# Kernel optimization log

Hardware: AMD Instinct MI355X
Metric: run time of the kernel (lower is better)

The kernel has to match this reference:

```python
import jax, jax.numpy as jnp
import numpy as np

N = 200000
E = 3200000
EPS = 1e-5


def setup_inputs() -> dict:
    key = jax.random.key(0)
    ks = jax.random.split(key, 8)
    x = jax.random.normal(ks[0], (N, 128), dtype=jnp.float32)
    edge_index = jax.random.randint(ks[1], (2, E), 0, N, dtype=jnp.int32)
    def lin(k, fi, fo):
        s = 1.0 / np.sqrt(fi)
        return jax.random.uniform(k, (fi, fo), jnp.float32, -s, s)
    return {
        "x": x,
        "edge_index": edge_index,
        "W1": lin(ks[2], 128, 256), "b1": jnp.zeros((256,), jnp.float32),
        "gamma1": jnp.ones((256,), jnp.float32), "beta1": jnp.zeros((256,), jnp.float32),
        "W2": lin(ks[3], 256, 256), "b2": jnp.zeros((256,), jnp.float32),
        "gamma2": jnp.ones((256,), jnp.float32), "beta2": jnp.zeros((256,), jnp.float32),
        "W3": lin(ks[4], 256, 40), "b3": jnp.zeros((40,), jnp.float32),
    }


def _gcn_norm(edge_index):
    # add self-loops, compute symmetric GCN normalization
    loop = jnp.arange(N, dtype=jnp.int32)
    row = jnp.concatenate([edge_index[0], loop])
    col = jnp.concatenate([edge_index[1], loop])
    deg = jax.ops.segment_sum(jnp.ones_like(row, dtype=jnp.float32), row, num_segments=N)
    dinv = jax.lax.rsqrt(jnp.maximum(deg, 1.0))  # deg >= 1 due to self-loops
    norm = dinv[row] * dinv[col]  # [E+N]
    return row, col, norm


def _gcn_conv(x, W, b, row, col, norm):
    h = x @ W                                  # [N, Fout] small GEMM
    msg = h[col] * norm[:, None]               # gather + scale  [E+N, Fout]
    out = jax.ops.segment_sum(msg, row, num_segments=N)  # scatter-add
    return out + b


def _batchnorm(x, gamma, beta):
    mu = jnp.mean(x, axis=0)
    var = jnp.var(x, axis=0)
    return (x - mu) * jax.lax.rsqrt(var + EPS) * gamma + beta


def reference(x, edge_index, W1, b1, gamma1, beta1, W2, b2, gamma2, beta2, W3, b3):
    row, col, norm = _gcn_norm(edge_index)
    h = _gcn_conv(x, W1, b1, row, col, norm)
    h = jax.nn.relu(_batchnorm(h, gamma1, beta1))
    h = _gcn_conv(h, W2, b2, row, col, norm)
    h = jax.nn.relu(_batchnorm(h, gamma2, beta2))
    h = _gcn_conv(h, W3, b3, row, col, norm)
    return jax.nn.log_softmax(h, axis=-1)
```

## Files before the change

### kernel.cpp

```cpp
#include <hip/hip_runtime.h>
#include <hip/hip_bf16.h>

#define NNODES 200000
#define NEDGES 3200000
#define NBUCK 782
#define NEB 512
#define EPB (NEDGES / NEB)
#define EPS 1e-5f
#define AGGB_CHUNK 50000
#define AGGF_CHUNK 100000

typedef __bf16 bf16x8 __attribute__((ext_vector_type(8)));
typedef float  f32x4  __attribute__((ext_vector_type(4)));
typedef float  f32x2  __attribute__((ext_vector_type(2)));

__device__ __forceinline__ float bflo(unsigned u) { return __uint_as_float(u << 16); }
__device__ __forceinline__ float bfhi(unsigned u) { return __uint_as_float(u & 0xffff0000u); }
__device__ __forceinline__ unsigned short f2b(float f) {
    return __builtin_bit_cast(unsigned short, __float2bfloat16(f));
}
__device__ __forceinline__ unsigned pk2(float a, float b) {
    return (unsigned)f2b(a) | ((unsigned)f2b(b) << 16);
}
__device__ __forceinline__ unsigned bnrelu_pk(unsigned u, f32x2 c, f32x2 h) {
    f32x2 v = { __uint_as_float(u << 16), __uint_as_float(u & 0xffff0000u) };
    v = __builtin_elementwise_fma(v, c, h);
    const f32x2 z = {0.f, 0.f};
    v = __builtin_elementwise_max(v, z);
    return pk2(v[0], v[1]);
}

__device__ __forceinline__ void prepw_one(const float* __restrict__ W,
                                          unsigned short* __restrict__ Wswz,
                                          int K, int NOUT, int t) {
    int KSTEPS = K / 32;
    int lane = t & 63;
    int ks = (t >> 6) % KSTEPS;
    int g  = (t >> 6) / KSTEPS;
    int c = lane & 15, q = lane >> 4;
    int col = g * 16 + c;
    int k0 = ks * 32 + q * 8;
    unsigned short vals[8];
#pragma unroll
    for (int j = 0; j < 8; ++j)
        vals[j] = (col < NOUT) ? f2b(W[(size_t)(k0 + j) * NOUT + col]) : (unsigned short)0;
    *(uint4*)((char*)Wswz + (size_t)t * 16) = __builtin_bit_cast(uint4, vals);
}

__global__ __launch_bounds__(256) void k_cnt(const int* __restrict__ row, int* __restrict__ cnt,
                                             const float* __restrict__ W1,
                                             const float* __restrict__ W2,
                                             const float* __restrict__ W3,
                                             unsigned short* __restrict__ w1s,
                                             unsigned short* __restrict__ w2s,
                                             unsigned short* __restrict__ w3s,
                                             unsigned* __restrict__ statsz) {
    const int blk = blockIdx.x;
    if (blk == NEB + 54) {
        for (int i = threadIdx.x; i < 1026; i += 256) statsz[i] = 0u;
        return;
    }
    if (blk >= NEB) {
        int t = (blk - NEB) * 256 + threadIdx.x;
        if (t < 4096) prepw_one(W1, w1s, 128, 256, t);
        else if (t < 12288) prepw_one(W2, w2s, 256, 256, t - 4096);
        else if (t < 13824) prepw_one(W3, w3s, 256, 40, t - 12288);
        return;
    }
    __shared__ int h[NBUCK];
    for (int i = threadIdx.x; i < NBUCK; i += 256) h[i] = 0;
    __syncthreads();
    const int e0 = blk * EPB;
    for (int i = e0 + threadIdx.x; i < e0 + EPB; i += 256)
        atomicAdd(&h[row[i] >> 8], 1);
    __syncthreads();
    for (int i = threadIdx.x; i < NBUCK; i += 256)
        cnt[(size_t)blk * NBUCK + i] = h[i];
}

__global__ __launch_bounds__(256) void k_bscan(int* __restrict__ cnt, int* __restrict__ btot) {
    const int wv = (blockIdx.x * 256 + threadIdx.x) >> 6;
    const int lane = threadIdx.x & 63;
    if (wv >= NBUCK) return;
    int v[8]; int s = 0;
#pragma unroll
    for (int j = 0; j < 8; ++j) {
        v[j] = cnt[(size_t)(lane * 8 + j) * NBUCK + wv];
        s += v[j];
    }
    int excl = s;
#pragma unroll
    for (int o = 1; o < 64; o <<= 1) {
        int t = __shfl_up(excl, o);
        if (lane >= o) excl += t;
    }
    excl -= s;
    if (lane == 63) btot[wv] = excl + s;
    int base = excl;
#pragma unroll
    for (int j = 0; j < 8; ++j) {
        int t = v[j];
        cnt[(size_t)(lane * 8 + j) * NBUCK + wv] = base;
        base += t;
    }
}

__global__ __launch_bounds__(256) void k_place(const int* __restrict__ row, const int* __restrict__ col,
                                               const int* __restrict__ cnt, const int* __restrict__ btot,
                                               int* __restrict__ bbase, unsigned* __restrict__ ebuf) {
    __shared__ int sbb[NBUCK];
    __shared__ int tp[256];
    __shared__ int base[NBUCK];
    const int t = threadIdx.x;
    int v[4]; int loc = 0;
    const int i0 = t * 4;
#pragma unroll
    for (int j = 0; j < 4; ++j) {
        int idx = i0 + j;
        v[j] = (idx < NBUCK) ? btot[idx] : 0;
        loc += v[j];
    }
    tp[t] = loc;
    __syncthreads();
    for (int off = 1; off < 256; off <<= 1) {
        int u = (t >= off) ? tp[t - off] : 0;
        __syncthreads();
        tp[t] += u;
        __syncthreads();
    }
    int run = tp[t] - loc;
#pragma unroll
    for (int j = 0; j < 4; ++j) {
        int idx = i0 + j;
        if (idx < NBUCK) sbb[idx] = run;
        run += v[j];
    }
    __syncthreads();
    if (blockIdx.x == 0) {
        for (int i = t; i < NBUCK; i += 256) bbase[i] = sbb[i];
        if (t == 0) bbase[NBUCK] = NEDGES;
    }
    for (int i = t; i < NBUCK; i += 256)
        base[i] = sbb[i] + cnt[(size_t)blockIdx.x * NBUCK + i];
    __syncthreads();
    const int e0 = blockIdx.x * EPB;
    for (int i = e0 + t; i < e0 + EPB; i += 256) {
        int r = row[i], c = col[i];
        int p = atomicAdd(&base[r >> 8], 1);
        ebuf[p] = ((unsigned)(r & 255) << 18) | (unsigned)c;
    }
}

__global__ __launch_bounds__(256) void k_sort2(const unsigned* __restrict__ ebuf,
                                               const int* __restrict__ bbase,
                                               int* __restrict__ offs, float* __restrict__ dinv,
                                               int* __restrict__ csr,
                                               const float* __restrict__ x,
                                               uint4* __restrict__ xb) {
    __shared__ int cnt[256];
    __shared__ int sofs[256];
    __shared__ int sc[256];
    __shared__ float sdinv[256];
    const int b = blockIdx.x;
    const int t = threadIdx.x;
    const int n0 = b * 256;
    cnt[t] = 0;
    __syncthreads();
    const int s = bbase[b], e = bbase[b + 1];
    for (int i = s + t; i < e; i += 256)
        atomicAdd(&cnt[ebuf[i] >> 18], 1);
    __syncthreads();
    const int c = cnt[t];
    sc[t] = c;
    __syncthreads();
    for (int off = 1; off < 256; off <<= 1) {
        int v = (t >= off) ? sc[t - off] : 0;
        __syncthreads();
        sc[t] += v;
        __syncthreads();
    }
    const int excl = sc[t] - c;
    sofs[t] = s + excl;
    const int n = n0 + t;
    float dv = rsqrtf((float)(c + 1));
    sdinv[t] = dv;
    if (n < NNODES) {
        offs[n] = s + excl;
        dinv[n] = dv;
    }
    if (b == NBUCK - 1 && t == 0) offs[NNODES] = NEDGES;
    cnt[t] = 0;
    __syncthreads();
    for (int i = s + t; i < e; i += 256) {
        unsigned v = ebuf[i];
        int nl = v >> 18;
        int rank = atomicAdd(&cnt[nl], 1);
        csr[sofs[nl] + rank] = (int)(v & 0x3FFFFu);
    }
    const int nn = (NNODES - n0 < 256) ? (NNODES - n0) : 256;
    const float4* xp = (const float4*)(x + (size_t)n0 * 128);
    uint4* xo = xb + (size_t)n0 * 16;
    const int lim = nn * 16;
    for (int i = t; i < lim; i += 256) {
        float d = sdinv[i >> 4];
        float4 a = xp[i * 2], bb = xp[i * 2 + 1];
        uint4 o;
        o.x = pk2(a.x * d, a.y * d);  o.y = pk2(a.z * d, a.w * d);
        o.z = pk2(bb.x * d, bb.y * d); o.w = pk2(bb.z * d, bb.w * d);
        xo[i] = o;
    }
}

__global__ __launch_bounds__(256) void k_aggf(const uint4* __restrict__ in,
                                              const int* __restrict__ offs,
                                              const int* __restrict__ csr,
                                              const float* __restrict__ dinv,
                                              uint4* __restrict__ out,
                                              int nbase) {
    const int lane = threadIdx.x & 63;
    const int grp = lane >> 4;
    const int fl = lane & 15;
    const int node = nbase + blockIdx.x * 4 + (threadIdx.x >> 6);
    const int p0 = offs[node];
    const int K = offs[node + 1] - p0 + 1;
    float a0=0,a1=0,a2=0,a3=0,a4=0,a5=0,a6=0,a7=0;
    auto accum = [&](uint4 u) {
        a0 += bflo(u.x); a1 += bfhi(u.x);
        a2 += bflo(u.y); a3 += bfhi(u.y);
        a4 += bflo(u.z); a5 += bfhi(u.z);
        a6 += bflo(u.w); a7 += bfhi(u.w);
    };
    int k = 0;
    for (; k + 16 <= K; k += 16) {
        int j0 = k + grp;
        int i0 = (j0 == 0) ? node : csr[p0 + j0 - 1];
        int i1 = csr[p0 + k + 3 + grp];
        int i2 = csr[p0 + k + 7 + grp];
        int i3 = csr[p0 + k + 11 + grp];
        uint4 u0 = in[(size_t)i0 * 16 + fl];
        uint4 u1 = in[(size_t)i1 * 16 + fl];
        uint4 u2 = in[(size_t)i2 * 16 + fl];
        uint4 u3 = in[(size_t)i3 * 16 + fl];
        accum(u0); accum(u1); accum(u2); accum(u3);
    }
    for (; k + 8 <= K; k += 8) {
        int j0 = k + grp;
        int i0 = (j0 == 0) ? node : csr[p0 + j0 - 1];
        int i1 = csr[p0 + k + 3 + grp];
        uint4 u0 = in[(size_t)i0 * 16 + fl];
        uint4 u1 = in[(size_t)i1 * 16 + fl];
        accum(u0); accum(u1);
    }
    for (; k + 4 <= K; k += 4) {
        int j0 = k + grp;
        int i0 = (j0 == 0) ? node : csr[p0 + j0 - 1];
        accum(in[(size_t)i0 * 16 + fl]);
    }
    int rem = K - k;
    if (grp < rem) {
        int j0 = k + grp;
        int i0 = (j0 == 0) ? node : csr[p0 + j0 - 1];
        accum(in[(size_t)i0 * 16 + fl]);
    }
#define RED(v) v += __shfl_xor(v, 32); v += __shfl_xor(v, 16);
    RED(a0) RED(a1) RED(a2) RED(a3) RED(a4) RED(a5) RED(a6) RED(a7)
#undef RED
    if (grp == 0) {
        const float d = dinv[node];
        uint4 o;
        o.x = pk2(a0 * d, a1 * d); o.y = pk2(a2 * d, a3 * d);
        o.z = pk2(a4 * d, a5 * d); o.w = pk2(a6 * d, a7 * d);
        out[(size_t)node * 16 + fl] = o;
    }
}

__global__ __launch_bounds__(256) void k_aggb(const uint4* __restrict__ in,
                                              const int* __restrict__ offs,
                                              const int* __restrict__ csr,
                                              const float* __restrict__ dinv,
                                              uint4* __restrict__ out,
                                              int nbase) {
    const int lane = threadIdx.x & 63;
    const int half = lane >> 5;
    const int fl = lane & 31;
    const int node = nbase + blockIdx.x * 4 + (threadIdx.x >> 6);
    const int p0 = offs[node];
    const int K = offs[node + 1] - p0 + 1;
    float a0=0,a1=0,a2=0,a3=0,a4=0,a5=0,a6=0,a7=0;
    auto accum = [&](uint4 u) {
        a0 += bflo(u.x); a1 += bfhi(u.x);
        a2 += bflo(u.y); a3 += bfhi(u.y);
        a4 += bflo(u.z); a5 += bfhi(u.z);
        a6 += bflo(u.w); a7 += bfhi(u.w);
    };
    auto idxAt = [&](int j) -> int { return (j == 0) ? node : csr[p0 + j - 1]; };
    int k = 0;
    for (; k + 8 <= K; k += 8) {
        int i0 = idxAt(k + half);
        int i1 = csr[p0 + k + 1 + half];
        int i2 = csr[p0 + k + 3 + half];
        int i3 = csr[p0 + k + 5 + half];
        uint4 u0 = in[(size_t)i0 * 32 + fl];
        uint4 u1 = in[(size_t)i1 * 32 + fl];
        uint4 u2 = in[(size_t)i2 * 32 + fl];
        uint4 u3 = in[(size_t)i3 * 32 + fl];
        accum(u0); accum(u1); accum(u2); accum(u3);
    }
    for (; k + 2 <= K; k += 2) {
        accum(in[(size_t)idxAt(k + half) * 32 + fl]);
    }
    if (k < K && half == 0) {
        accum(in[(size_t)idxAt(k) * 32 + fl]);
    }
#define RED(v) v += __shfl_xor(v, 32);
    RED(a0) RED(a1) RED(a2) RED(a3) RED(a4) RED(a5) RED(a6) RED(a7)
#undef RED
    if (half == 0) {
        const float d = dinv[node];
        uint4 o;
        o.x = pk2(a0 * d, a1 * d); o.y = pk2(a2 * d, a3 * d);
        o.z = pk2(a4 * d, a5 * d); o.w = pk2(a6 * d, a7 * d);
        out[(size_t)node * 32 + fl] = o;
    }
}

__global__ __launch_bounds__(256) void k_agg3(const uint4* __restrict__ T3b,
                                              const int* __restrict__ offs,
                                              const int* __restrict__ csr,
                                              const float* __restrict__ dinv,
                                              const float* __restrict__ b3,
                                              float* __restrict__ out) {
    const int lane = threadIdx.x & 63;
    const int grp = lane / 5;
    const int fl = lane - grp * 5;
    const bool act = grp < 12;
    const int node = blockIdx.x * 4 + (threadIdx.x >> 6);
    const int p0 = offs[node];
    const int K = offs[node + 1] - p0 + 1;
    float a0=0,a1=0,a2=0,a3=0,a4=0,a5=0,a6=0,a7=0;
    auto accum = [&](uint4 u) {
        a0 += bflo(u.x); a1 += bfhi(u.x);
        a2 += bflo(u.y); a3 += bfhi(u.y);
        a4 += bflo(u.z); a5 += bfhi(u.z);
        a6 += bflo(u.w); a7 += bfhi(u.w);
    };
    const char* Tb = (const char*)T3b;
    int k = 0;
    if (act) {
        for (; k + 12 <= K; k += 12) {
            int j = k + grp;
            int i0 = (j == 0) ? node : csr[p0 + j - 1];
            accum(*(const uint4*)(Tb + (size_t)i0 * 128 + fl * 16));
        }
        int rem = K - k;
        if (grp < rem) {
            int j = k + grp;
            int i0 = (j == 0) ? node : csr[p0 + j - 1];
            accum(*(const uint4*)(Tb + (size_t)i0 * 128 + fl * 16));
        }
    }
#define RED3(v) { float t = __shfl(v, lane + 30); v += t; t = __shfl(v, lane + 15); v += t; \
                  float u1 = __shfl(v, lane + 5); float u2 = __shfl(v, lane + 10); v += u1 + u2; }
    RED3(a0) RED3(a1) RED3(a2) RED3(a3) RED3(a4) RED3(a5) RED3(a6) RED3(a7)
#undef RED3
    const float d = dinv[node];
    float v[8];
    if (grp == 0) {
        const float4* bp = (const float4*)(b3 + fl * 8);
        float4 b01 = bp[0], b23 = bp[1];
        v[0] = a0 * d + b01.x; v[1] = a1 * d + b01.y;
        v[2] = a2 * d + b01.z; v[3] = a3 * d + b01.w;
        v[4] = a4 * d + b23.x; v[5] = a5 * d + b23.y;
        v[6] = a6 * d + b23.z; v[7] = a7 * d + b23.w;
    } else {
#pragma unroll
        for (int j = 0; j < 8; ++j) v[j] = -INFINITY;
    }
    float m = v[0];
#pragma unroll
    for (int j = 1; j < 8; ++j) m = fmaxf(m, v[j]);
    float mm = __shfl(m, 0);
#pragma unroll
    for (int l = 1; l < 5; ++l) mm = fmaxf(mm, __shfl(m, l));
    float e = 0.f;
    if (grp == 0) {
#pragma unroll
        for (int j = 0; j < 8; ++j) e += __expf(v[j] - mm);
    }
    float s = __shfl(e, 0);
#pragma unroll
    for (int l = 1; l < 5; ++l) s += __shfl(e, l);
    float ls = __logf(s);
    if (grp == 0) {
        float* op = out + (size_t)node * 40 + fl * 8;
        float4 o0 = {v[0] - mm - ls, v[1] - mm - ls, v[2] - mm - ls, v[3] - mm - ls};
        float4 o1 = {v[4] - mm - ls, v[5] - mm - ls, v[6] - mm - ls, v[7] - mm - ls};
        *(float4*)op = o0;
        *(float4*)(op + 4) = o1;
    }
}

template <int K, int MW, int NW, int WNB, bool PRESCALE, bool BNA, bool STATS>
__global__ __launch_bounds__(MW * NW * 64) void k_gemm(const __hip_bfloat16* __restrict__ A,
                                                       const __hip_bfloat16* __restrict__ Wswz,
                                                       const float* __restrict__ dinvp,
                                                       const float* __restrict__ bnsc,
                                                       const float* __restrict__ bnsh,
                                                       unsigned short* __restrict__ Cout,
                                                       int M, int NOUT, int CS,
                                                       float* __restrict__ sums,
                                                       float* __restrict__ sq,
                                                       const float* __restrict__ gamma,
                                                       const float* __restrict__ beta,
                                                       float* __restrict__ scale,
                                                       float* __restrict__ shift,
                                                       int* __restrict__ done) {
    constexpr int KSTEPS = K / 32;
    constexpr int NTHR   = MW * NW * 64;
    constexpr int ROWS   = MW * 64;
    constexpr int STAGE_U4 = (ROWS * 64) / (NTHR * 16);
    __shared__ __align__(16) unsigned short As[2][ROWS * 32];

    const int t = threadIdx.x;
    const int lane = t & 63;
    const int wid  = t >> 6;
    const int wm = (wid % MW) * 64;
    const int wn = (wid / MW) * (WNB * 16);
    const long rowBase = (long)blockIdx.x * ROWS;
    const int cl = lane & 15, q = lane >> 4;
    const int colq = t & 3;

    const __hip_bfloat16* bptr[WNB];
#pragma unroll
    for (int nf = 0; nf < WNB; ++nf) {
        int g = wn / 16 + nf;
        bptr[nf] = Wswz + (size_t)g * KSTEPS * 512 + (size_t)lane * 8;
    }

    uint4 stg[STAGE_U4];
    auto stage_ld = [&](int ks) {
#pragma unroll
        for (int u = 0; u < STAGE_U4; ++u) {
            int rg = (t >> 2) + u * (NTHR >> 2);
            long r = rowBase + rg; if (r > M - 1) r = M - 1;
            stg[u] = *(const uint4*)((const char*)A + (size_t)r * (K * 2) + ks * 64 + colq * 16);
        }
    };
    auto stage_st = [&](int ks, int bsel) {
        f32x2 cp[4], hp[4];
        if constexpr (BNA) {
            const f32x2* cpp = (const f32x2*)(bnsc + ks * 32 + colq * 8);
            const f32x2* hpp = (const f32x2*)(bnsh + ks * 32 + colq * 8);
#pragma unroll
            for (int j = 0; j < 4; ++j) { cp[j] = cpp[j]; hp[j] = hpp[j]; }
        }
#pragma unroll
        for (int u = 0; u < STAGE_U4; ++u) {
            uint4 v = stg[u];
            if constexpr (BNA) {
                v.x = bnrelu_pk(v.x, cp[0], hp[0]);
                v.y = bnrelu_pk(v.y, cp[1], hp[1]);
                v.z = bnrelu_pk(v.z, cp[2], hp[2]);
                v.w = bnrelu_pk(v.w, cp[3], hp[3]);
            }
            int rg = (t >> 2) + u * (NTHR >> 2);
            *(uint4*)&As[bsel][rg * 32 + colq * 8] = v;
        }
    };

    f32x4 acc[4][WNB];
    const f32x4 z = {0.f, 0.f, 0.f, 0.f};
#pragma unroll
    for (int mf = 0; mf < 4; ++mf)
#pragma unroll
        for (int nf = 0; nf < WNB; ++nf) acc[mf][nf] = z;

    stage_ld(0);
    stage_st(0, 0);
    __syncthreads();

#pragma unroll
    for (int ks = 0; ks < KSTEPS; ++ks) {
        const int cur = ks & 1;
        if (ks + 1 < KSTEPS) stage_ld(ks + 1);
        bf16x8 a[4], b[WNB];
#pragma unroll
        for (int nf = 0; nf < WNB; ++nf)
            b[nf] = __builtin_bit_cast(bf16x8, *(const uint4*)(bptr[nf] + ks * 512));
#pragma unroll
        for (int mf = 0; mf < 4; ++mf)
            a[mf] = __builtin_bit_cast(bf16x8, *(const uint4*)&As[cur][(wm + mf * 16 + cl) * 32 + q * 8]);
#pragma unroll
        for (int mf = 0; mf < 4; ++mf)
#pragma unroll
            for (int nf = 0; nf < WNB; ++nf)
                acc[mf][nf] = __builtin_amdgcn_mfma_f32_16x16x32_bf16(a[mf], b[nf], acc[mf][nf], 0, 0, 0);
        if (ks + 1 < KSTEPS) {
            stage_st(ks + 1, cur ^ 1);
            __syncthreads();
        }
    }

#pragma unroll
    for (int mf = 0; mf < 4; ++mf)
#pragma unroll
        for (int i = 0; i < 4; ++i) {
            long row = rowBase + wm + mf * 16 + q * 4 + i;
            if (row >= M) continue;
            float dv = PRESCALE ? dinvp[row] : 1.0f;
#pragma unroll
            for (int nf = 0; nf < WNB; ++nf) {
                int col = wn + nf * 16 + cl;
                if (col < NOUT)
                    Cout[row * CS + col] = f2b(PRESCALE ? acc[mf][nf][i] * dv : acc[mf][nf][i]);
            }
        }

    if constexpr (STATS) {
#pragma unroll
        for (int nf = 0; nf < WNB; ++nf) {
            float s = 0.f, s2 = 0.f;
#pragma unroll
            for (int mf = 0; mf < 4; ++mf)
#pragma unroll
                for (int i = 0; i < 4; ++i) {
                    long row = rowBase + wm + mf * 16 + q * 4 + i;
                    float v = (row < M) ? acc[mf][nf][i] : 0.f;
                    s += v; s2 += v * v;
                }
            s  += __shfl_xor(s, 16);  s  += __shfl_xor(s, 32);
            s2 += __shfl_xor(s2, 16); s2 += __shfl_xor(s2, 32);
            if (q == 0) {
                int col = wn + nf * 16 + cl;
                if (col < NOUT) {
                    atomicAdd(&sums[col], s);
                    atomicAdd(&sq[col], s2);
                }
            }
        }
        __syncthreads();
        __shared__ int lastf;
        if (threadIdx.x == 0) lastf = (atomicAdd(done, 1) == (int)gridDim.x - 1) ? 1 : 0;
        __syncthreads();
        if (lastf) {
            const int tt = threadIdx.x;
            float su = atomicAdd(&sums[tt], 0.0f);
            float qu = atomicAdd(&sq[tt], 0.0f);
            float mu = su * (1.0f / NNODES);
            float var = qu * (1.0f / NNODES) - mu * mu;
            if (var < 0.f) var = 0.f;
            float sc = gamma[tt] * rsqrtf(var + EPS);
            scale[tt] = sc;
            shift[tt] = beta[tt] - mu * sc;
        }
    }
}

__global__ __launch_bounds__(256) void k_stats(const uint4* __restrict__ Zu,
                                               float* __restrict__ sums, float* __restrict__ sq,
                                               const float* __restrict__ gamma,
                                               const float* __restrict__ beta,
                                               float* __restrict__ scale, float* __restrict__ shift,
                                               int* __restrict__ done) {
    __shared__ float reds[8][256];
    __shared__ float redq[8][256];
    const int t = threadIdx.x;
    const int cg = t & 31;
    const int rs = t >> 5;
    const long r0 = (long)blockIdx.x * 256 + (long)rs * 32;
    float s[8], q[8];
#pragma unroll
    for (int j = 0; j < 8; ++j) { s[j] = 0.f; q[j] = 0.f; }
    for (int i = 0; i < 32; ++i) {
        long r = r0 + i;
        if (r >= NNODES) break;
        uint4 u = Zu[r * 32 + cg];
        float v0 = bflo(u.x), v1 = bfhi(u.x), v2 = bflo(u.y), v3 = bfhi(u.y);
        float v4 = bflo(u.z), v5 = bfhi(u.z), v6 = bflo(u.w), v7 = bfhi(u.w);
        s[0] += v0; q[0] += v0 * v0;  s[1] += v1; q[1] += v1 * v1;
        s[2] += v2; q[2] += v2 * v2;  s[3] += v3; q[3] += v3 * v3;
        s[4] += v4; q[4] += v4 * v4;  s[5] += v5; q[5] += v5 * v5;
        s[6] += v6; q[6] += v6 * v6;  s[7] += v7; q[7] += v7 * v7;
    }
#pragma unroll
    for (int j = 0; j < 8; ++j) {
        reds[rs][cg * 8 + j] = s[j];
        redq[rs][cg * 8 + j] = q[j];
    }
    __syncthreads();
    float S = 0.f, Q = 0.f;
#pragma unroll
    for (int j = 0; j < 8; ++j) { S += reds[j][t]; Q += redq[j][t]; }
    atomicAdd(&sums[t], S);
    atomicAdd(&sq[t], Q);
    __syncthreads();
    __shared__ int lastf;
    if (t == 0) lastf = (atomicAdd(done, 1) == (int)gridDim.x - 1) ? 1 : 0;
    __syncthreads();
    if (lastf) {
        float su = atomicAdd(&sums[t], 0.0f);
        float qu = atomicAdd(&sq[t], 0.0f);
        float mu = su * (1.0f / NNODES);
        float var = qu * (1.0f / NNODES) - mu * mu;
        if (var < 0.f) var = 0.f;
        float sc = gamma[t] * rsqrtf(var + EPS);
        scale[t] = sc;
        shift[t] = beta[t] - mu * sc;
    }
}

extern "C" void kernel_launch(void* const* d_in, const int* in_sizes, int n_in,
                              void* d_out, int out_size, void* d_ws, size_t ws_size,
                              hipStream_t stream) {
    const float* x   = (const float*)d_in[0];
    const int*   ei  = (const int*)d_in[1];
    const float* W1  = (const float*)d_in[2];
    const float* g1  = (const float*)d_in[4];
    const float* be1 = (const float*)d_in[5];
    const float* W2  = (const float*)d_in[6];
    const float* g2  = (const float*)d_in[8];
    const float* be2 = (const float*)d_in[9];
    const float* W3  = (const float*)d_in[10];
    const float* b3  = (const float*)d_in[11];

    char* w = (char*)d_ws;
    size_t o = 0;
    auto alloc = [&](size_t b) { size_t r = o; o += (b + 255) & ~(size_t)255; return r; };
    int*   offs = (int*)(w + alloc((size_t)(NNODES + 1) * 4));
    float* dinv = (float*)(w + alloc((size_t)NNODES * 4));
    int*   cnt  = (int*)(w + alloc((size_t)NEB * NBUCK * 4));
    int*   btot = (int*)(w + alloc(NBUCK * 4));
    int*   bbase= (int*)(w + alloc((NBUCK + 1) * 4));
    unsigned* ebuf = (unsigned*)(w + alloc((size_t)NEDGES * 4));
    int*   csr  = (int*)(w + alloc((size_t)NEDGES * 4));
    float* stats = (float*)(w + alloc(4 * 256 * 4 + 32));
    float* bnp   = (float*)(w + alloc(4 * 256 * 4));
    unsigned short* w1s = (unsigned short*)(w + alloc(65536));
    unsigned short* w2s = (unsigned short*)(w + alloc(131072));
    unsigned short* w3s = (unsigned short*)(w + alloc(24576));
    __hip_bfloat16* xb   = (__hip_bfloat16*)(w + alloc((size_t)NNODES * 128 * 2));
    __hip_bfloat16* buf0 = (__hip_bfloat16*)(w + alloc((size_t)NNODES * 128 * 2));
    __hip_bfloat16* buf1 = (__hip_bfloat16*)(w + alloc((size_t)NNODES * 256 * 2));
    __hip_bfloat16* buf2 = (__hip_bfloat16*)(w + alloc((size_t)NNODES * 256 * 2));

    float* sums1 = stats;       float* sq1 = stats + 256;
    float* sums2 = stats + 512; float* sq2 = stats + 768;
    int*   done1 = (int*)(stats + 1024);
    int*   done2 = done1 + 1;
    float* scale1 = bnp;        float* shift1 = bnp + 256;
    float* scale2 = bnp + 512;  float* shift2 = bnp + 768;

    const int SB = (NNODES + 255) / 256;

    k_cnt<<<NEB + 55, 256, 0, stream>>>(ei, cnt, W1, W2, W3, w1s, w2s, w3s, (unsigned*)stats);
    k_bscan<<<(NBUCK * 64 + 255) / 256, 256, 0, stream>>>(cnt, btot);
    k_place<<<NEB, 256, 0, stream>>>(ei, ei + NEDGES, cnt, btot, bbase, ebuf);
    k_sort2<<<NBUCK, 256, 0, stream>>>(ebuf, bbase, offs, dinv, csr, x, (uint4*)xb);

    const dim3 g64((NNODES + 63) / 64, 1);

    for (int c = 0; c < 2; ++c)
        k_aggf<<<AGGF_CHUNK / 4, 256, 0, stream>>>((const uint4*)xb, offs, csr, dinv, (uint4*)buf0, c * AGGF_CHUNK);
    k_gemm<128, 1, 4, 4, false, false, true><<<g64, 256, 0, stream>>>(buf0, (const __hip_bfloat16*)w1s, nullptr, nullptr, nullptr, (unsigned short*)buf1, NNODES, 256, 256, sums1, sq1, g1, be1, scale1, shift1, done1);

    k_gemm<256, 1, 4, 4, true, true, false><<<g64, 256, 0, stream>>>(buf1, (const __hip_bfloat16*)w2s, dinv, scale1, shift1, (unsigned short*)buf2, NNODES, 256, 256, nullptr, nullptr, nullptr, nullptr, nullptr, nullptr, nullptr);
    for (int c = 0; c < 4; ++c)
        k_aggb<<<AGGB_CHUNK / 4, 256, 0, stream>>>((const uint4*)buf2, offs, csr, dinv, (uint4*)buf1, c * AGGB_CHUNK);
    k_stats<<<SB, 256, 0, stream>>>((const uint4*)buf1, sums2, sq2, g2, be2, scale2, shift2, done2);

    k_gemm<256, 4, 1, 3, true, true, false><<<dim3((NNODES + 255) / 256, 1), 256, 0, stream>>>(buf1, (const __hip_bfloat16*)w3s, dinv, scale2, shift2, (unsigned short*)buf0, NNODES, 40, 64, nullptr, nullptr, nullptr, nullptr, nullptr, nullptr, nullptr);
    k_agg3<<<NNODES / 4, 256, 0, stream>>>((const uint4*)buf0, offs, csr, dinv, b3, (float*)d_out);
}
```

Measured before the change: 1.042 ms.

## Stage full-K A tile in LDS once and unify GEMM tiling to 64-row blocks

The GEMM kernel no longer double-buffers A across K-steps. Each block now loads its whole 64-row by K tile into padded LDS in one pass, with BN+ReLU applied once per element, and then runs all MFMA steps without per-step barriers. The third GEMM moves from a 256-row, 4-wave-in-M layout to 64-row blocks with 4 waves split over N (WNB=1, 64 padded columns), so the W3 swizzle buffer and prep blocks grow. This removes per-K syncs and the staging pipeline, at the cost of more LDS per block and no overlap of global loads with compute. The row clamp is dropped, which relies on NNODES being a multiple of 64.

```diff
diff --git a/kernel.cpp b/kernel.cpp
--- a/kernel.cpp
+++ b/kernel.cpp
@@ -56,7 +56,7 @@
                                              unsigned short* __restrict__ w3s,
                                              unsigned* __restrict__ statsz) {
     const int blk = blockIdx.x;
-    if (blk == NEB + 54) {
+    if (blk == NEB + 56) {
         for (int i = threadIdx.x; i < 1026; i += 256) statsz[i] = 0u;
         return;
     }
@@ -64,7 +64,7 @@
         int t = (blk - NEB) * 256 + threadIdx.x;
         if (t < 4096) prepw_one(W1, w1s, 128, 256, t);
         else if (t < 12288) prepw_one(W2, w2s, 256, 256, t - 4096);
-        else if (t < 13824) prepw_one(W3, w3s, 256, 40, t - 12288);
+        else if (t < 14336) prepw_one(W3, w3s, 256, 40, t - 12288);
         return;
     }
     __shared__ int h[NBUCK];
@@ -400,73 +400,68 @@
     }
 }
 
-template <int K, int MW, int NW, int WNB, bool PRESCALE, bool BNA, bool STATS>
-__global__ __launch_bounds__(MW * NW * 64) void k_gemm(const __hip_bfloat16* __restrict__ A,
-                                                       const __hip_bfloat16* __restrict__ Wswz,
-                                                       const float* __restrict__ dinvp,
-                                                       const float* __restrict__ bnsc,
-                                                       const float* __restrict__ bnsh,
-                                                       unsigned short* __restrict__ Cout,
-                                                       int M, int NOUT, int CS,
-                                                       float* __restrict__ sums,
-                                                       float* __restrict__ sq,
-                                                       const float* __restrict__ gamma,
-                                                       const float* __restrict__ beta,
-                                                       float* __restrict__ scale,
-                                                       float* __restrict__ shift,
-                                                       int* __restrict__ done) {
+template <int K, int WNB, bool PRESCALE, bool BNA, bool STATS>
+__global__ __launch_bounds__(256) void k_gemm(const __hip_bfloat16* __restrict__ A,
+                                              const __hip_bfloat16* __restrict__ Wswz,
+                                              const float* __restrict__ dinvp,
+                                              const float* __restrict__ bnsc,
+                                              const float* __restrict__ bnsh,
+                                              unsigned short* __restrict__ Cout,
+                                              int M, int NOUT, int CS,
+                                              float* __restrict__ sums,
+                                              float* __restrict__ sq,
+                                              const float* __restrict__ gamma,
+                                              const float* __restrict__ beta,
+                                              float* __restrict__ scale,
+                                              float* __restrict__ shift,
+                                              int* __restrict__ done) {
     constexpr int KSTEPS = K / 32;
-    constexpr int NTHR   = MW * NW * 64;
-    constexpr int ROWS   = MW * 64;
-    constexpr int STAGE_U4 = (ROWS * 64) / (NTHR * 16);
-    __shared__ __align__(16) unsigned short As[2][ROWS * 32];
+    constexpr int LROW   = K + 8;
+    constexpr int U4R    = K / 8;
+    constexpr int NU     = K / 32;
+    constexpr int RPU    = 256 / U4R;
+    __shared__ __align__(16) unsigned short As[64 * LROW];
 
     const int t = threadIdx.x;
     const int lane = t & 63;
     const int wid  = t >> 6;
-    const int wm = (wid % MW) * 64;
-    const int wn = (wid / MW) * (WNB * 16);
-    const long rowBase = (long)blockIdx.x * ROWS;
+    const int wn = wid * (WNB * 16);
+    const long rowBase = (long)blockIdx.x * 64;
     const int cl = lane & 15, q = lane >> 4;
-    const int colq = t & 3;
+
+    const int cst = t % U4R;
+    const int r0l = t / U4R;
+    f32x2 cp[4], hp[4];
+    if constexpr (BNA) {
+        const f32x2* cpp = (const f32x2*)(bnsc + cst * 8);
+        const f32x2* hpp = (const f32x2*)(bnsh + cst * 8);
+#pragma unroll
+        for (int j = 0; j < 4; ++j) { cp[j] = cpp[j]; hp[j] = hpp[j]; }
+    }
+    uint4 stg[NU];
+#pragma unroll
+    for (int u = 0; u < NU; ++u) {
+        int rl = r0l + u * RPU;
+        stg[u] = *(const uint4*)((const char*)A + (size_t)(rowBase + rl) * (K * 2) + (size_t)cst * 16);
+    }
+#pragma unroll
+    for (int u = 0; u < NU; ++u) {
+        uint4 v = stg[u];
+        if constexpr (BNA) {
+            v.x = bnrelu_pk(v.x, cp[0], hp[0]);
+            v.y = bnrelu_pk(v.y, cp[1], hp[1]);
+            v.z = bnrelu_pk(v.z, cp[2], hp[2]);
+            v.w = bnrelu_pk(v.w, cp[3], hp[3]);
+        }
+        int rl = r0l + u * RPU;
+        *(uint4*)&As[rl * LROW + cst * 8] = v;
+    }
+    __syncthreads();
 
     const __hip_bfloat16* bptr[WNB];
 #pragma unroll
-    for (int nf = 0; nf < WNB; ++nf) {
-        int g = wn / 16 + nf;
-        bptr[nf] = Wswz + (size_t)g * KSTEPS * 512 + (size_t)lane * 8;
-    }
-
-    uint4 stg[STAGE_U4];
-    auto stage_ld = [&](int ks) {
-#pragma unroll
-        for (int u = 0; u < STAGE_U4; ++u) {
-            int rg = (t >> 2) + u * (NTHR >> 2);
-            long r = rowBase + rg; if (r > M - 1) r = M - 1;
-            stg[u] = *(const uint4*)((const char*)A + (size_t)r * (K * 2) + ks * 64 + colq * 16);
-        }
-    };
-    auto stage_st = [&](int ks, int bsel) {
-        f32x2 cp[4], hp[4];
-        if constexpr (BNA) {
-            const f32x2* cpp = (const f32x2*)(bnsc + ks * 32 + colq * 8);
-            const f32x2* hpp = (const f32x2*)(bnsh + ks * 32 + colq * 8);
-#pragma unroll
-            for (int j = 0; j < 4; ++j) { cp[j] = cpp[j]; hp[j] = hpp[j]; }
-        }
-#pragma unroll
-        for (int u = 0; u < STAGE_U4; ++u) {
-            uint4 v = stg[u];
-            if constexpr (BNA) {
-                v.x = bnrelu_pk(v.x, cp[0], hp[0]);
-                v.y = bnrelu_pk(v.y, cp[1], hp[1]);
-                v.z = bnrelu_pk(v.z, cp[2], hp[2]);
-                v.w = bnrelu_pk(v.w, cp[3], hp[3]);
-            }
-            int rg = (t >> 2) + u * (NTHR >> 2);
-            *(uint4*)&As[bsel][rg * 32 + colq * 8] = v;
-        }
-    };
+    for (int nf = 0; nf < WNB; ++nf)
+        bptr[nf] = Wswz + (size_t)(wn / 16 + nf) * KSTEPS * 512 + (size_t)lane * 8;
 
     f32x4 acc[4][WNB];
     const f32x4 z = {0.f, 0.f, 0.f, 0.f};
@@ -475,37 +470,27 @@
 #pragma unroll
         for (int nf = 0; nf < WNB; ++nf) acc[mf][nf] = z;
 
-    stage_ld(0);
-    stage_st(0, 0);
-    __syncthreads();
-
 #pragma unroll
     for (int ks = 0; ks < KSTEPS; ++ks) {
-        const int cur = ks & 1;
-        if (ks + 1 < KSTEPS) stage_ld(ks + 1);
         bf16x8 a[4], b[WNB];
 #pragma unroll
         for (int nf = 0; nf < WNB; ++nf)
             b[nf] = __builtin_bit_cast(bf16x8, *(const uint4*)(bptr[nf] + ks * 512));
 #pragma unroll
         for (int mf = 0; mf < 4; ++mf)
-            a[mf] = __builtin_bit_cast(bf16x8, *(const uint4*)&As[cur][(wm + mf * 16 + cl) * 32 + q * 8]);
+            a[mf] = __builtin_bit_cast(bf16x8, *(const uint4*)&As[(mf * 16 + cl) * LROW + ks * 32 + q * 8]);
 #pragma unroll
         for (int mf = 0; mf < 4; ++mf)
 #pragma unroll
             for (int nf = 0; nf < WNB; ++nf)
                 acc[mf][nf] = __builtin_amdgcn_mfma_f32_16x16x32_bf16(a[mf], b[nf], acc[mf][nf], 0, 0, 0);
-        if (ks + 1 < KSTEPS) {
-            stage_st(ks + 1, cur ^ 1);
-            __syncthreads();
-        }
     }
 
 #pragma unroll
     for (int mf = 0; mf < 4; ++mf)
 #pragma unroll
         for (int i = 0; i < 4; ++i) {
-            long row = rowBase + wm + mf * 16 + q * 4 + i;
+            long row = rowBase + mf * 16 + q * 4 + i;
             if (row >= M) continue;
             float dv = PRESCALE ? dinvp[row] : 1.0f;
 #pragma unroll
@@ -524,7 +509,7 @@
             for (int mf = 0; mf < 4; ++mf)
 #pragma unroll
                 for (int i = 0; i < 4; ++i) {
-                    long row = rowBase + wm + mf * 16 + q * 4 + i;
+                    long row = rowBase + mf * 16 + q * 4 + i;
                     float v = (row < M) ? acc[mf][nf][i] : 0.f;
                     s += v; s2 += v * v;
                 }
@@ -637,7 +622,7 @@
     float* bnp   = (float*)(w + alloc(4 * 256 * 4));
     unsigned short* w1s = (unsigned short*)(w + alloc(65536));
     unsigned short* w2s = (unsigned short*)(w + alloc(131072));
-    unsigned short* w3s = (unsigned short*)(w + alloc(24576));
+    unsigned short* w3s = (unsigned short*)(w + alloc(32768));
     __hip_bfloat16* xb   = (__hip_bfloat16*)(w + alloc((size_t)NNODES * 128 * 2));
     __hip_bfloat16* buf0 = (__hip_bfloat16*)(w + alloc((size_t)NNODES * 128 * 2));
     __hip_bfloat16* buf1 = (__hip_bfloat16*)(w + alloc((size_t)NNODES * 256 * 2));
@@ -651,23 +636,22 @@
     float* scale2 = bnp + 512;  float* shift2 = bnp + 768;
 
     const int SB = (NNODES + 255) / 256;
-
-    k_cnt<<<NEB + 55, 256, 0, stream>>>(ei, cnt, W1, W2, W3, w1s, w2s, w3s, (unsigned*)stats);
+    const int GB = NNODES / 64;
+
+    k_cnt<<<NEB + 57, 256, 0, stream>>>(ei, cnt, W1, W2, W3, w1s, w2s, w3s, (unsigned*)stats);
     k_bscan<<<(NBUCK * 64 + 255) / 256, 256, 0, stream>>>(cnt, btot);
     k_place<<<NEB, 256, 0, stream>>>(ei, ei + NEDGES, cnt, btot, bbase, ebuf);
     k_sort2<<<NBUCK, 256, 0, stream>>>(ebuf, bbase, offs, dinv, csr, x, (uint4*)xb);
 
-    const dim3 g64((NNODES + 63) / 64, 1);
-
     for (int c = 0; c < 2; ++c)
         k_aggf<<<AGGF_CHUNK / 4, 256, 0, stream>>>((const uint4*)xb, offs, csr, dinv, (uint4*)buf0, c * AGGF_CHUNK);
-    k_gemm<128, 1, 4, 4, false, false, true><<<g64, 256, 0, stream>>>(buf0, (const __hip_bfloat16*)w1s, nullptr, nullptr, nullptr, (unsigned short*)buf1, NNODES, 256, 256, sums1, sq1, g1, be1, scale1, shift1, done1);
-
-    k_gemm<256, 1, 4, 4, true, true, false><<<g64, 256, 0, stream>>>(buf1, (const __hip_bfloat16*)w2s, dinv, scale1, shift1, (unsigned short*)buf2, NNODES, 256, 256, nullptr, nullptr, nullptr, nullptr, nullptr, nullptr, nullptr);
+    k_gemm<128, 4, false, false, true><<<GB, 256, 0, stream>>>(buf0, (const __hip_bfloat16*)w1s, nullptr, nullptr, nullptr, (unsigned short*)buf1, NNODES, 256, 256, sums1, sq1, g1, be1, scale1, shift1, done1);
+
+    k_gemm<256, 4, true, true, false><<<GB, 256, 0, stream>>>(buf1, (const __hip_bfloat16*)w2s, dinv, scale1, shift1, (unsigned short*)buf2, NNODES, 256, 256, nullptr, nullptr, nullptr, nullptr, nullptr, nullptr, nullptr);
     for (int c = 0; c < 4; ++c)
         k_aggb<<<AGGB_CHUNK / 4, 256, 0, stream>>>((const uint4*)buf2, offs, csr, dinv, (uint4*)buf1, c * AGGB_CHUNK);
     k_stats<<<SB, 256, 0, stream>>>((const uint4*)buf1, sums2, sq2, g2, be2, scale2, shift2, done2);
 
-    k_gemm<256, 4, 1, 3, true, true, false><<<dim3((NNODES + 255) / 256, 1), 256, 0, stream>>>(buf1, (const __hip_bfloat16*)w3s, dinv, scale2, shift2, (unsigned short*)buf0, NNODES, 40, 64, nullptr, nullptr, nullptr, nullptr, nullptr, nullptr, nullptr);
+    k_gemm<256, 1, true, true, false><<<GB, 256, 0, stream>>>(buf1, (const __hip_bfloat16*)w3s, dinv, scale2, shift2, (unsigned short*)buf0, NNODES, 40, 64, nullptr, nullptr, nullptr, nullptr, nullptr, nullptr, nullptr);
     k_agg3<<<NNODES / 4, 256, 0, stream>>>((const uint4*)buf0, offs, csr, dinv, b3, (float*)d_out);
 }
```

After: 1.010 ms. 1.03x faster.
